# Performance work log

Hardware: AMD Instinct MI355X
Metric: run time of the kernel (lower is better)

## Reference

```python
import jax, jax.numpy as jnp
import numpy as np

C_SKIP = 64       # channels of a and of b (concat -> 128)
C_OUT = 64
N = 131072        # coarse nodes
E = 1048576       # directed edges (avg degree 8)
N_FINE = 4 * N    # fine mesh nodes after unpool
K = 3 * N_FINE    # unpool scatter assignments


def setup_inputs() -> dict:
    key = jax.random.key(0)
    ks = jax.random.split(key, 9)
    return {
        "a": jax.random.normal(ks[0], (C_SKIP, N), dtype=jnp.float32),
        "b": jax.random.normal(ks[1], (C_SKIP, N), dtype=jnp.float32),
        "W_self": jax.random.normal(ks[2], (C_OUT, 2 * C_SKIP), dtype=jnp.float32) * 0.05,
        "W_neigh": jax.random.normal(ks[3], (C_OUT, 2 * C_SKIP), dtype=jnp.float32) * 0.05,
        "bias": jax.random.normal(ks[4], (C_OUT,), dtype=jnp.float32) * 0.05,
        "gather_index": jax.random.randint(ks[5], (E,), 0, N),
        "reduce_index": jax.random.randint(ks[6], (E,), 0, N),
        "unpool_src": jax.random.randint(ks[7], (K,), 0, N),
        "unpool_dst": jax.random.randint(ks[8], (K,), 0, N_FINE),
    }


def reference(a, b, W_self, W_neigh, bias, gather_index, reduce_index, unpool_src, unpool_dst):
    # concat skip connection along channel dim (-2)
    x = jnp.concatenate((a, b), axis=-2)                  # [C_in, N]
    n = x.shape[-1]
    # GraphConv: gather source features along edges, segment-sum into targets
    msgs = x[:, gather_index]                              # [C_in, E]
    agg = jax.ops.segment_sum(msgs.T, reduce_index, num_segments=n).T  # [C_in, N]
    h = W_self @ x + W_neigh @ agg + bias[:, None]         # [C_out, N]
    h = jax.nn.relu(h)
    # GraphUnpool with reduce='amax': scatter-max coarse features to fine mesh
    out = jnp.zeros((h.shape[0], 4 * n), dtype=h.dtype)
    out = out.at[:, unpool_dst].max(h[:, unpool_src])      # [C_out, N_fine]
    return out
```

## Files before the change

### kernel.cpp

```cpp
#include <hip/hip_runtime.h>
#include <stdint.h>

constexpr int NN = 131072;
constexpr int EE = 1048576;
constexpr int NF = 4 * NN;
constexpr int KK = 3 * NF;

constexpr int NSB  = 256;
constexpr int TPS  = 1024;
constexpr int SHC_E = 9;
constexpr int SHC_K = 10;
constexpr int NBC_E = NN >> SHC_E;
constexpr int NBC_K = NF >> SHC_K;
constexpr int EPT_E = EE / NSB / TPS;
constexpr int EPT_K = KK / NSB / TPS;
constexpr int KOFF2 = NBC_E * NSB;
constexpr int NH2   = KOFF2 + NBC_K * NSB;
constexpr int NSCB  = NH2 / 2048;
constexpr int NTRB  = NN / 32 / 4;

constexpr int CAP_AG = 1024;
constexpr int CAP_UP = 896;

typedef __attribute__((ext_vector_type(8))) short bf16x8;
typedef __attribute__((ext_vector_type(4))) float f32x4;

__device__ inline uint32_t bf16rn(float f) {
    uint32_t u = __float_as_uint(f);
    return (u + 0x7FFFu + ((u >> 16) & 1u)) >> 16;
}
__device__ inline uint32_t pack2(float lo, float hi) {
    return bf16rn(lo) | (bf16rn(hi) << 16);
}
__device__ inline float bf_lo(uint32_t v) { return __uint_as_float(v << 16); }
__device__ inline float bf_hi(uint32_t v) { return __uint_as_float(v & 0xFFFF0000u); }

template<int NB, int EPT>
__device__ void pass1_body(const int* __restrict__ idx, int shift,
                           int* __restrict__ histG, int blk, int* hist)
{
    for (int f = threadIdx.x; f < NB; f += TPS) hist[f] = 0;
    __syncthreads();
    int base = blk * (TPS * EPT);
#pragma unroll
    for (int u = 0; u < EPT; ++u) {
        int b = idx[base + u * TPS + threadIdx.x] >> shift;
        atomicAdd(&hist[b], 1);
    }
    __syncthreads();
    for (int f = threadIdx.x; f < NB; f += TPS)
        histG[f * NSB + blk] = hist[f];
}

__global__ __launch_bounds__(1024) void k_fused1(
    const float* __restrict__ a, const float* __restrict__ b,
    uint32_t* __restrict__ xTb,
    const int* __restrict__ reduce_i, const int* __restrict__ up_dst,
    int* __restrict__ histG)
{
    __shared__ int smem[128 * 33];
    if (blockIdx.x < NTRB) {
        float (*tile)[33] = (float (*)[33])smem;
        for (int t = 0; t < 4; ++t) {
            int i0 = (blockIdx.x * 4 + t) * 32;
            for (int f = threadIdx.x; f < 128 * 32; f += TPS) {
                int c = f >> 5, j = f & 31;
                const float* src = (c < 64) ? a : b;
                tile[c][j] = src[(size_t)(c & 63) * NN + i0 + j];
            }
            __syncthreads();
            for (int f = threadIdx.x; f < 64 * 32; f += TPS) {
                int p = f & 63, j = f >> 6;
                xTb[(size_t)(i0 + j) * 64 + p] =
                    pack2(tile[2 * p][j], tile[2 * p + 1][j]);
            }
            __syncthreads();
        }
    } else if (blockIdx.x < NTRB + NSB) {
        pass1_body<NBC_E, EPT_E>(reduce_i, SHC_E, histG, blockIdx.x - NTRB, smem);
    } else {
        pass1_body<NBC_K, EPT_K>(up_dst, SHC_K, histG + KOFF2,
                                 blockIdx.x - NTRB - NSB, smem);
    }
}

__global__ __launch_bounds__(256) void k_bsum(
    const int* __restrict__ cnt, int* __restrict__ bsum)
{
    __shared__ int s[256];
    int base = blockIdx.x * 2048;
    int sum = 0;
    for (int j = threadIdx.x; j < 2048; j += 256) sum += cnt[base + j];
    s[threadIdx.x] = sum;
    __syncthreads();
    for (int o = 128; o > 0; o >>= 1) {
        if (threadIdx.x < o) s[threadIdx.x] += s[threadIdx.x + o];
        __syncthreads();
    }
    if (threadIdx.x == 0) bsum[blockIdx.x] = s[0];
}

__global__ __launch_bounds__(256) void k_final(
    int* __restrict__ offs, const int* __restrict__ bsum)
{
    __shared__ int ts[256];
    int partial = 0;
    for (int i = threadIdx.x; i < blockIdx.x; i += 256) partial += bsum[i];
    ts[threadIdx.x] = partial;
    __syncthreads();
    for (int o = 128; o > 0; o >>= 1) {
        if (threadIdx.x < o) ts[threadIdx.x] += ts[threadIdx.x + o];
        __syncthreads();
    }
    int bb = ts[0];
    __syncthreads();

    int base = blockIdx.x * 2048 + threadIdx.x * 8;
    int loc[8];
    int sum = 0;
#pragma unroll
    for (int u = 0; u < 8; ++u) {
        int v = offs[base + u];
        loc[u] = sum;
        sum += v;
    }
    ts[threadIdx.x] = sum;
    __syncthreads();
    for (int o = 1; o < 256; o <<= 1) {
        int v = (threadIdx.x >= o) ? ts[threadIdx.x - o] : 0;
        __syncthreads();
        ts[threadIdx.x] += v;
        __syncthreads();
    }
    int texc = (threadIdx.x == 0) ? 0 : ts[threadIdx.x - 1];
#pragma unroll
    for (int u = 0; u < 8; ++u) offs[base + u] = bb + texc + loc[u];
    if (blockIdx.x == gridDim.x - 1 && threadIdx.x == 255) offs[NH2] = bb + ts[255];
}

template<int NB, int EPT>
__device__ void pass2_body(const int* __restrict__ idx,
                           const int* __restrict__ payload, int shift,
                           const int* __restrict__ offsG, int sub,
                           uint32_t* __restrict__ pairs, int blk, int* curs)
{
    int lmask = (1 << shift) - 1;
    for (int f = threadIdx.x; f < NB; f += TPS)
        curs[f] = offsG[f * NSB + blk] - sub;
    __syncthreads();
    int base = blk * (TPS * EPT);
#pragma unroll
    for (int u = 0; u < EPT; ++u) {
        int e = base + u * TPS + threadIdx.x;
        int bk = idx[e];
        int pos = atomicAdd(&curs[bk >> shift], 1);
        pairs[pos] = (uint32_t)payload[e] | ((uint32_t)(bk & lmask) << 17);
    }
}

__global__ __launch_bounds__(1024) void k_pass2(
    const int* __restrict__ reduce_i, const int* __restrict__ gather_i,
    const int* __restrict__ up_dst, const int* __restrict__ up_src,
    const int* __restrict__ offs,
    uint32_t* __restrict__ pairsE, uint32_t* __restrict__ pairsK)
{
    __shared__ int curs[NBC_K];
    if (blockIdx.x < NSB)
        pass2_body<NBC_E, EPT_E>(reduce_i, gather_i, SHC_E, offs, 0,
                                 pairsE, blockIdx.x, curs);
    else
        pass2_body<NBC_K, EPT_K>(up_dst, up_src, SHC_K, offs + KOFF2, EE,
                                 pairsK, blockIdx.x - NSB, curs);
}

__global__ __launch_bounds__(256) void k_aggcsr(
    const uint32_t* __restrict__ xTb, const int* __restrict__ offs,
    const uint32_t* __restrict__ pairsE, uint32_t* __restrict__ aggB)
{
    __shared__ uint32_t stage[CAP_AG];
    __shared__ uint32_t list[CAP_AG];
    __shared__ int loffs[65];
    __shared__ int curs[64];
    __shared__ int nstage;
    int binc = blockIdx.x >> 3, sub = blockIdx.x & 7;
    int beg = offs[binc * NSB], end = offs[(binc + 1) * NSB];
    if (threadIdx.x == 0) nstage = 0;
    if (threadIdx.x < 64) curs[threadIdx.x] = 0;
    __syncthreads();
    int lane = threadIdx.x & 63;

    for (int i0 = beg; i0 < end; i0 += 256) {
        int i = i0 + threadIdx.x;
        bool mine = false;
        uint32_t ent = 0;
        if (i < end) {
            uint32_t u = pairsE[i];
            int loc = u >> 17;
            mine = (loc >> 6) == sub;
            ent = (u & 0x1FFFFu) | ((uint32_t)(loc & 63) << 17);
        }
        unsigned long long mask = __ballot(mine);
        if (mask) {
            int leader = __ffsll(mask) - 1;
            int rank = __popcll(mask & ((1ull << lane) - 1ull));
            int wb = 0;
            if (lane == leader) wb = atomicAdd(&nstage, (int)__popcll(mask));
            wb = __shfl(wb, leader);
            int p = wb + rank;
            if (mine && p < CAP_AG) stage[p] = ent;
        }
    }
    __syncthreads();
    int cnt = min(nstage, CAP_AG);
    for (int i = threadIdx.x; i < cnt; i += 256)
        atomicAdd(&curs[stage[i] >> 17], 1);
    __syncthreads();
    if (threadIdx.x == 0) {
        int run = 0;
        for (int j = 0; j < 64; ++j) {
            loffs[j] = run;
            run += curs[j];
            curs[j] = loffs[j];
        }
        loffs[64] = run;
    }
    __syncthreads();
    for (int i = threadIdx.x; i < cnt; i += 256) {
        uint32_t u = stage[i];
        int p = atomicAdd(&curs[u >> 17], 1);
        list[p] = u;
    }
    __syncthreads();

    int w = threadIdx.x >> 6;
    int n0 = w * 16, n1 = n0 + 16;
    int e0 = loffs[n0], e1 = loffs[n1];
    size_t rowbase = (size_t)(binc * 512 + sub * 64) * 64 + lane;
    float sx = 0.f, sy = 0.f;
    int cur = n0;
    for (int e = e0; e < e1; e += 16) {
        int nb = e1 - e;
        uint32_t pr[16], v[16];
#pragma unroll
        for (int j = 0; j < 16; ++j)
            pr[j] = list[e + ((j < nb) ? j : (nb - 1))];
#pragma unroll
        for (int j = 0; j < 16; ++j)
            v[j] = xTb[(size_t)(pr[j] & 0x1FFFF) * 64 + lane];
#pragma unroll
        for (int j = 0; j < 16; ++j) {
            if (j < nb) {
                int d = pr[j] >> 17;
                if (d != cur) {
                    aggB[rowbase + (size_t)cur * 64] = pack2(sx, sy);
                    for (int z = cur + 1; z < d; ++z)
                        aggB[rowbase + (size_t)z * 64] = 0u;
                    cur = d;
                    sx = 0.f; sy = 0.f;
                }
                sx += bf_lo(v[j]);
                sy += bf_hi(v[j]);
            }
        }
    }
    aggB[rowbase + (size_t)cur * 64] = pack2(sx, sy);
    for (int z = cur + 1; z < n1; ++z)
        aggB[rowbase + (size_t)z * 64] = 0u;
}

__global__ __launch_bounds__(256) void k_gemm(
    const uint32_t* __restrict__ xTb, const uint32_t* __restrict__ aggB,
    const float* __restrict__ Wself, const float* __restrict__ Wneigh,
    const float* __restrict__ bias, uint32_t* __restrict__ hT)
{
    int lane = threadIdx.x & 63;
    int wid = blockIdx.x * 4 + (threadIdx.x >> 6);
    int lr = lane & 15, lq = lane >> 4;

    bf16x8 wf[4][8];
#pragma unroll
    for (int mt = 0; mt < 4; ++mt) {
#pragma unroll
        for (int kt = 0; kt < 8; ++kt) {
            const float* W = (kt < 4) ? Wself : Wneigh;
            const float* p = W + (size_t)(mt * 16 + lr) * 128 + (kt & 3) * 32 + lq * 8;
            bf16x8 v;
#pragma unroll
            for (int j = 0; j < 8; ++j) v[j] = (short)bf16rn(p[j]);
            wf[mt][kt] = v;
        }
    }
    float bv[4][4];
#pragma unroll
    for (int mt = 0; mt < 4; ++mt)
#pragma unroll
        for (int r = 0; r < 4; ++r)
            bv[mt][r] = bias[mt * 16 + lq * 4 + r];

    const int NG = NN / 16;
    int stride = gridDim.x * 4;
    for (int g = wid; g < NG; g += stride) {
        int n = g * 16 + lr;
        const uint32_t* xr = xTb + (size_t)n * 64 + lq * 4;
        const uint32_t* ar = aggB + (size_t)n * 64 + lq * 4;
        bf16x8 bq[8];
#pragma unroll
        for (int kt = 0; kt < 4; ++kt)
            bq[kt] = *reinterpret_cast<const bf16x8*>(xr + kt * 16);
#pragma unroll
        for (int kt = 0; kt < 4; ++kt)
            bq[4 + kt] = *reinterpret_cast<const bf16x8*>(ar + kt * 16);
#pragma unroll
        for (int mt = 0; mt < 4; ++mt) {
            f32x4 acc = {0.f, 0.f, 0.f, 0.f};
#pragma unroll
            for (int kt = 0; kt < 8; ++kt)
                acc = __builtin_amdgcn_mfma_f32_16x16x32_bf16(wf[mt][kt], bq[kt], acc, 0, 0, 0);
            uint32_t u0 = pack2(fmaxf(acc[0] + bv[mt][0], 0.f), fmaxf(acc[1] + bv[mt][1], 0.f));
            uint32_t u1 = pack2(fmaxf(acc[2] + bv[mt][2], 0.f), fmaxf(acc[3] + bv[mt][3], 0.f));
            *reinterpret_cast<uint2*>(hT + (size_t)n * 32 + mt * 8 + lq * 2) = make_uint2(u0, u1);
        }
    }
}

__global__ __launch_bounds__(256) void k_unpoolcsr(
    const uint16_t* __restrict__ hT16, const int* __restrict__ offsK,
    const uint32_t* __restrict__ pairsK, float* __restrict__ out)
{
    __shared__ uint32_t stage[CAP_UP];
    __shared__ uint32_t list[CAP_UP];
    __shared__ int loffs[129];
    __shared__ int curs[128];
    __shared__ uint16_t buf[128][65];
    __shared__ int nstage;
    int binc = blockIdx.x >> 3, sub = blockIdx.x & 7;
    int beg = offsK[binc * NSB] - EE, end = offsK[(binc + 1) * NSB] - EE;
    if (threadIdx.x == 0) nstage = 0;
    if (threadIdx.x < 128) curs[threadIdx.x] = 0;
    for (int f = threadIdx.x; f < 128 * 65; f += 256) ((uint16_t*)buf)[f] = 0;
    __syncthreads();
    int lane = threadIdx.x & 63;

    for (int i0 = beg; i0 < end; i0 += 256) {
        int i = i0 + threadIdx.x;
        bool mine = false;
        uint32_t ent = 0;
        if (i < end) {
            uint32_t u = pairsK[i];
            int loc = u >> 17;
            mine = (loc >> 7) == sub;
            ent = (u & 0x1FFFFu) | ((uint32_t)(loc & 127) << 17);
        }
        unsigned long long mask = __ballot(mine);
        if (mask) {
            int leader = __ffsll(mask) - 1;
            int rank = __popcll(mask & ((1ull << lane) - 1ull));
            int wb = 0;
            if (lane == leader) wb = atomicAdd(&nstage, (int)__popcll(mask));
            wb = __shfl(wb, leader);
            int p = wb + rank;
            if (mine && p < CAP_UP) stage[p] = ent;
        }
    }
    __syncthreads();
    int cnt = min(nstage, CAP_UP);
    for (int i = threadIdx.x; i < cnt; i += 256)
        atomicAdd(&curs[stage[i] >> 17], 1);
    __syncthreads();
    if (threadIdx.x == 0) {
        int run = 0;
        for (int j = 0; j < 128; ++j) {
            loffs[j] = run;
            run += curs[j];
            curs[j] = loffs[j];
        }
        loffs[128] = run;
    }
    __syncthreads();
    for (int i = threadIdx.x; i < cnt; i += 256) {
        uint32_t u = stage[i];
        int p = atomicAdd(&curs[u >> 17], 1);
        list[p] = u;
    }
    __syncthreads();

    int w = threadIdx.x >> 6;
    int n0 = w * 32, n1 = n0 + 32;
    int e0 = loffs[n0], e1 = loffs[n1];
    uint32_t m = 0;
    int cur = n0;
    for (int e = e0; e < e1; e += 16) {
        int nb = e1 - e;
        uint32_t pr[16], v[16];
#pragma unroll
        for (int j = 0; j < 16; ++j)
            pr[j] = list[e + ((j < nb) ? j : (nb - 1))];
#pragma unroll
        for (int j = 0; j < 16; ++j)
            v[j] = hT16[(size_t)(pr[j] & 0x1FFFF) * 64 + lane];
#pragma unroll
        for (int j = 0; j < 16; ++j) {
            if (j < nb) {
                int d = pr[j] >> 17;
                if (d != cur) {
                    buf[cur][lane] = (uint16_t)m;
                    cur = d;
                    m = 0;
                }
                m = max(m, v[j]);
            }
        }
    }
    buf[cur][lane] = (uint16_t)m;
    __syncthreads();
    int j0 = binc * 1024 + sub * 128;
    for (int f = threadIdx.x; f < 64 * 128; f += 256) {
        int c = f >> 7, j = f & 127;
        out[(size_t)c * NF + j0 + j] = __uint_as_float(((uint32_t)buf[j][c]) << 16);
    }
}

extern "C" void kernel_launch(void* const* d_in, const int* in_sizes, int n_in,
                              void* d_out, int out_size, void* d_ws, size_t ws_size,
                              hipStream_t stream)
{
    const float* a      = (const float*)d_in[0];
    const float* b      = (const float*)d_in[1];
    const float* Wself  = (const float*)d_in[2];
    const float* Wneigh = (const float*)d_in[3];
    const float* bias   = (const float*)d_in[4];
    const int* gather_i = (const int*)d_in[5];
    const int* reduce_i = (const int*)d_in[6];
    const int* up_src   = (const int*)d_in[7];
    const int* up_dst   = (const int*)d_in[8];
    float* out = (float*)d_out;

    uint32_t* xTb   = (uint32_t*)d_ws;
    uint32_t* aggB  = xTb + (size_t)NN * 64;
    uint32_t* hT    = aggB + (size_t)NN * 64;
    uint32_t* pairsK= hT + (size_t)NN * 32;
    int* offs       = (int*)(pairsK + KK);
    int* bsum       = offs + (size_t)NH2 + 1;
    uint32_t* pairsE= hT;

    size_t need = ((size_t)NN * 160 + KK + (size_t)NH2 + 1 + NSCB) * 4;
    if (ws_size < need) return;

    k_fused1<<<NTRB + 2 * NSB, TPS, 0, stream>>>(a, b, xTb, reduce_i, up_dst, offs);

    k_bsum<<<NSCB, 256, 0, stream>>>(offs, bsum);
    k_final<<<NSCB, 256, 0, stream>>>(offs, bsum);

    k_pass2<<<2 * NSB, TPS, 0, stream>>>(reduce_i, gather_i, up_dst, up_src,
                                         offs, pairsE, pairsK);

    k_aggcsr<<<8 * NBC_E, 256, 0, stream>>>(xTb, offs, pairsE, aggB);

    k_gemm<<<512, 256, 0, stream>>>(xTb, aggB, Wself, Wneigh, bias, hT);

    k_unpoolcsr<<<8 * NBC_K, 256, 0, stream>>>((const uint16_t*)hT, offs + KOFF2,
                                               pairsK, out);
}
```

Before: 243.3 us.

## Add per-bucket node-level sort pass to build full CSR offsets

Adds a new k_pass3 kernel that sorts each coarse bucket's pairs by local node in place and writes global per-node offset arrays for both the edge and unpool lists. The aggregation and unpool kernels then read their node ranges directly from these offsets. Before, each of eight sub-blocks rescanned the whole bucket, filtered it with ballots and ran a serial single-thread prefix scan. This removes that eightfold redundant scanning and the per-block local sort, at the cost of one extra launch and more workspace for the offset arrays.

```diff
diff --git a/kernel.cpp b/kernel.cpp
--- a/kernel.cpp
+++ b/kernel.cpp
@@ -19,8 +19,8 @@
 constexpr int NSCB  = NH2 / 2048;
 constexpr int NTRB  = NN / 32 / 4;
 
-constexpr int CAP_AG = 1024;
-constexpr int CAP_UP = 896;
+constexpr int CAP3_E = 5120;
+constexpr int CAP3_K = 4096;
 
 typedef __attribute__((ext_vector_type(8))) short bf16x8;
 typedef __attribute__((ext_vector_type(4))) float f32x4;
@@ -173,77 +173,82 @@
                                  pairsK, blockIdx.x - NSB, curs);
 }
 
-__global__ __launch_bounds__(256) void k_aggcsr(
-    const uint32_t* __restrict__ xTb, const int* __restrict__ offs,
+template<int NB, int CAP>
+__device__ void pass3_body(uint32_t* __restrict__ pairs, int beg, int end,
+                           int* __restrict__ nodeOff, int nodeBase,
+                           bool last, int totalNode,
+                           uint32_t* list, int* curs, int* tmp)
+{
+    int tid = threadIdx.x;
+    int cnt = min(end - beg, CAP);
+    for (int i = tid; i < cnt; i += TPS) list[i] = pairs[beg + i];
+    if (tid < NB) curs[tid] = 0;
+    __syncthreads();
+    for (int i = tid; i < cnt; i += TPS) atomicAdd(&curs[list[i] >> 17], 1);
+    __syncthreads();
+    int own = (tid < NB) ? curs[tid] : 0;
+    if (tid < NB) tmp[tid] = own;
+    __syncthreads();
+    for (int o = 1; o < NB; o <<= 1) {
+        int v = (tid < NB && tid >= o) ? tmp[tid - o] : 0;
+        __syncthreads();
+        if (tid < NB) tmp[tid] += v;
+        __syncthreads();
+    }
+    if (tid < NB) {
+        int excl = tmp[tid] - own;
+        curs[tid] = excl;
+        nodeOff[nodeBase + tid] = beg + excl;
+    }
+    if (last && tid == 0) nodeOff[totalNode] = beg + cnt;
+    __syncthreads();
+    for (int i = tid; i < cnt; i += TPS) {
+        uint32_t u = list[i];
+        int p = atomicAdd(&curs[u >> 17], 1);
+        pairs[beg + p] = u;
+    }
+}
+
+__global__ __launch_bounds__(1024) void k_pass3(
+    const int* __restrict__ offs,
+    uint32_t* __restrict__ pairsE, uint32_t* __restrict__ pairsK,
+    int* __restrict__ nodeOffE, int* __restrict__ nodeOffK)
+{
+    __shared__ uint32_t list[CAP3_E];
+    __shared__ int curs[1024];
+    __shared__ int tmp[1024];
+    if (blockIdx.x < NBC_E) {
+        int b = blockIdx.x;
+        int beg = offs[b * NSB], end = offs[(b + 1) * NSB];
+        pass3_body<512, CAP3_E>(pairsE, beg, end, nodeOffE, b * 512,
+                                b == NBC_E - 1, NN, list, curs, tmp);
+    } else {
+        int b = blockIdx.x - NBC_E;
+        int beg = offs[KOFF2 + b * NSB] - EE;
+        int end = offs[KOFF2 + (b + 1) * NSB] - EE;
+        pass3_body<1024, CAP3_K>(pairsK, beg, end, nodeOffK, b * 1024,
+                                 b == NBC_K - 1, NF, list, curs, tmp);
+    }
+}
+
+__global__ __launch_bounds__(256) void k_agg2(
+    const uint32_t* __restrict__ xTb, const int* __restrict__ nodeOffE,
     const uint32_t* __restrict__ pairsE, uint32_t* __restrict__ aggB)
 {
-    __shared__ uint32_t stage[CAP_AG];
-    __shared__ uint32_t list[CAP_AG];
-    __shared__ int loffs[65];
-    __shared__ int curs[64];
-    __shared__ int nstage;
-    int binc = blockIdx.x >> 3, sub = blockIdx.x & 7;
-    int beg = offs[binc * NSB], end = offs[(binc + 1) * NSB];
-    if (threadIdx.x == 0) nstage = 0;
-    if (threadIdx.x < 64) curs[threadIdx.x] = 0;
-    __syncthreads();
-    int lane = threadIdx.x & 63;
-
-    for (int i0 = beg; i0 < end; i0 += 256) {
-        int i = i0 + threadIdx.x;
-        bool mine = false;
-        uint32_t ent = 0;
-        if (i < end) {
-            uint32_t u = pairsE[i];
-            int loc = u >> 17;
-            mine = (loc >> 6) == sub;
-            ent = (u & 0x1FFFFu) | ((uint32_t)(loc & 63) << 17);
-        }
-        unsigned long long mask = __ballot(mine);
-        if (mask) {
-            int leader = __ffsll(mask) - 1;
-            int rank = __popcll(mask & ((1ull << lane) - 1ull));
-            int wb = 0;
-            if (lane == leader) wb = atomicAdd(&nstage, (int)__popcll(mask));
-            wb = __shfl(wb, leader);
-            int p = wb + rank;
-            if (mine && p < CAP_AG) stage[p] = ent;
-        }
-    }
-    __syncthreads();
-    int cnt = min(nstage, CAP_AG);
-    for (int i = threadIdx.x; i < cnt; i += 256)
-        atomicAdd(&curs[stage[i] >> 17], 1);
-    __syncthreads();
-    if (threadIdx.x == 0) {
-        int run = 0;
-        for (int j = 0; j < 64; ++j) {
-            loffs[j] = run;
-            run += curs[j];
-            curs[j] = loffs[j];
-        }
-        loffs[64] = run;
-    }
-    __syncthreads();
-    for (int i = threadIdx.x; i < cnt; i += 256) {
-        uint32_t u = stage[i];
-        int p = atomicAdd(&curs[u >> 17], 1);
-        list[p] = u;
-    }
-    __syncthreads();
-
-    int w = threadIdx.x >> 6;
-    int n0 = w * 16, n1 = n0 + 16;
-    int e0 = loffs[n0], e1 = loffs[n1];
-    size_t rowbase = (size_t)(binc * 512 + sub * 64) * 64 + lane;
+    int w = threadIdx.x >> 6, lane = threadIdx.x & 63;
+    int n0g = blockIdx.x * 64 + w * 16;
+    int e0 = nodeOffE[n0g], e1 = nodeOffE[n0g + 16];
+    int curLoc = n0g & 511;
+    int curEnd = curLoc + 16;
+    int cbase = n0g - curLoc;
     float sx = 0.f, sy = 0.f;
-    int cur = n0;
+    int cur = curLoc;
     for (int e = e0; e < e1; e += 16) {
         int nb = e1 - e;
         uint32_t pr[16], v[16];
 #pragma unroll
         for (int j = 0; j < 16; ++j)
-            pr[j] = list[e + ((j < nb) ? j : (nb - 1))];
+            pr[j] = pairsE[e + ((j < nb) ? j : (nb - 1))];
 #pragma unroll
         for (int j = 0; j < 16; ++j)
             v[j] = xTb[(size_t)(pr[j] & 0x1FFFF) * 64 + lane];
@@ -252,9 +257,9 @@
             if (j < nb) {
                 int d = pr[j] >> 17;
                 if (d != cur) {
-                    aggB[rowbase + (size_t)cur * 64] = pack2(sx, sy);
+                    aggB[(size_t)(cbase + cur) * 64 + lane] = pack2(sx, sy);
                     for (int z = cur + 1; z < d; ++z)
-                        aggB[rowbase + (size_t)z * 64] = 0u;
+                        aggB[(size_t)(cbase + z) * 64 + lane] = 0u;
                     cur = d;
                     sx = 0.f; sy = 0.f;
                 }
@@ -263,9 +268,9 @@
             }
         }
     }
-    aggB[rowbase + (size_t)cur * 64] = pack2(sx, sy);
-    for (int z = cur + 1; z < n1; ++z)
-        aggB[rowbase + (size_t)z * 64] = 0u;
+    aggB[(size_t)(cbase + cur) * 64 + lane] = pack2(sx, sy);
+    for (int z = cur + 1; z < curEnd; ++z)
+        aggB[(size_t)(cbase + z) * 64 + lane] = 0u;
 }
 
 __global__ __launch_bounds__(256) void k_gemm(
@@ -323,85 +328,33 @@
     }
 }
 
-__global__ __launch_bounds__(256) void k_unpoolcsr(
-    const uint16_t* __restrict__ hT16, const int* __restrict__ offsK,
+__global__ __launch_bounds__(256) void k_unpool2(
+    const uint16_t* __restrict__ hT16, const int* __restrict__ nodeOffK,
     const uint32_t* __restrict__ pairsK, float* __restrict__ out)
 {
-    __shared__ uint32_t stage[CAP_UP];
-    __shared__ uint32_t list[CAP_UP];
-    __shared__ int loffs[129];
-    __shared__ int curs[128];
     __shared__ uint16_t buf[128][65];
-    __shared__ int nstage;
-    int binc = blockIdx.x >> 3, sub = blockIdx.x & 7;
-    int beg = offsK[binc * NSB] - EE, end = offsK[(binc + 1) * NSB] - EE;
-    if (threadIdx.x == 0) nstage = 0;
-    if (threadIdx.x < 128) curs[threadIdx.x] = 0;
+    int w = threadIdx.x >> 6, lane = threadIdx.x & 63;
+    int j0 = blockIdx.x * 128;
+    int lbase = j0 & 1023;
     for (int f = threadIdx.x; f < 128 * 65; f += 256) ((uint16_t*)buf)[f] = 0;
     __syncthreads();
-    int lane = threadIdx.x & 63;
-
-    for (int i0 = beg; i0 < end; i0 += 256) {
-        int i = i0 + threadIdx.x;
-        bool mine = false;
-        uint32_t ent = 0;
-        if (i < end) {
-            uint32_t u = pairsK[i];
-            int loc = u >> 17;
-            mine = (loc >> 7) == sub;
-            ent = (u & 0x1FFFFu) | ((uint32_t)(loc & 127) << 17);
-        }
-        unsigned long long mask = __ballot(mine);
-        if (mask) {
-            int leader = __ffsll(mask) - 1;
-            int rank = __popcll(mask & ((1ull << lane) - 1ull));
-            int wb = 0;
-            if (lane == leader) wb = atomicAdd(&nstage, (int)__popcll(mask));
-            wb = __shfl(wb, leader);
-            int p = wb + rank;
-            if (mine && p < CAP_UP) stage[p] = ent;
-        }
-    }
-    __syncthreads();
-    int cnt = min(nstage, CAP_UP);
-    for (int i = threadIdx.x; i < cnt; i += 256)
-        atomicAdd(&curs[stage[i] >> 17], 1);
-    __syncthreads();
-    if (threadIdx.x == 0) {
-        int run = 0;
-        for (int j = 0; j < 128; ++j) {
-            loffs[j] = run;
-            run += curs[j];
-            curs[j] = loffs[j];
-        }
-        loffs[128] = run;
-    }
-    __syncthreads();
-    for (int i = threadIdx.x; i < cnt; i += 256) {
-        uint32_t u = stage[i];
-        int p = atomicAdd(&curs[u >> 17], 1);
-        list[p] = u;
-    }
-    __syncthreads();
-
-    int w = threadIdx.x >> 6;
-    int n0 = w * 32, n1 = n0 + 32;
-    int e0 = loffs[n0], e1 = loffs[n1];
+    int n0 = j0 + w * 32;
+    int e0 = nodeOffK[n0], e1 = nodeOffK[n0 + 32];
     uint32_t m = 0;
-    int cur = n0;
+    int cur = (n0 & 1023) - lbase;
     for (int e = e0; e < e1; e += 16) {
         int nb = e1 - e;
         uint32_t pr[16], v[16];
 #pragma unroll
         for (int j = 0; j < 16; ++j)
-            pr[j] = list[e + ((j < nb) ? j : (nb - 1))];
+            pr[j] = pairsK[e + ((j < nb) ? j : (nb - 1))];
 #pragma unroll
         for (int j = 0; j < 16; ++j)
             v[j] = hT16[(size_t)(pr[j] & 0x1FFFF) * 64 + lane];
 #pragma unroll
         for (int j = 0; j < 16; ++j) {
             if (j < nb) {
-                int d = pr[j] >> 17;
+                int d = (int)(pr[j] >> 17) - lbase;
                 if (d != cur) {
                     buf[cur][lane] = (uint16_t)m;
                     cur = d;
@@ -413,7 +366,6 @@
     }
     buf[cur][lane] = (uint16_t)m;
     __syncthreads();
-    int j0 = binc * 1024 + sub * 128;
     for (int f = threadIdx.x; f < 64 * 128; f += 256) {
         int c = f >> 7, j = f & 127;
         out[(size_t)c * NF + j0 + j] = __uint_as_float(((uint32_t)buf[j][c]) << 16);
@@ -435,15 +387,18 @@
     const int* up_dst   = (const int*)d_in[8];
     float* out = (float*)d_out;
 
-    uint32_t* xTb   = (uint32_t*)d_ws;
-    uint32_t* aggB  = xTb + (size_t)NN * 64;
-    uint32_t* hT    = aggB + (size_t)NN * 64;
-    uint32_t* pairsK= hT + (size_t)NN * 32;
-    int* offs       = (int*)(pairsK + KK);
-    int* bsum       = offs + (size_t)NH2 + 1;
-    uint32_t* pairsE= hT;
-
-    size_t need = ((size_t)NN * 160 + KK + (size_t)NH2 + 1 + NSCB) * 4;
+    uint32_t* xTb    = (uint32_t*)d_ws;
+    uint32_t* aggB   = xTb + (size_t)NN * 64;
+    uint32_t* hT     = aggB + (size_t)NN * 64;
+    uint32_t* pairsK = hT + (size_t)NN * 32;
+    int* offs        = (int*)(pairsK + KK);
+    int* bsum        = offs + (size_t)NH2 + 1;
+    int* nodeOffE    = bsum + NSCB;
+    int* nodeOffK    = nodeOffE + NN + 1;
+    uint32_t* pairsE = hT;
+
+    size_t need = ((size_t)NN * 160 + KK + (size_t)NH2 + 1 + NSCB +
+                   (size_t)NN + 1 + (size_t)NF + 1) * 4;
     if (ws_size < need) return;
 
     k_fused1<<<NTRB + 2 * NSB, TPS, 0, stream>>>(a, b, xTb, reduce_i, up_dst, offs);
@@ -454,10 +409,13 @@
     k_pass2<<<2 * NSB, TPS, 0, stream>>>(reduce_i, gather_i, up_dst, up_src,
                                          offs, pairsE, pairsK);
 
-    k_aggcsr<<<8 * NBC_E, 256, 0, stream>>>(xTb, offs, pairsE, aggB);
+    k_pass3<<<NBC_E + NBC_K, TPS, 0, stream>>>(offs, pairsE, pairsK,
+                                               nodeOffE, nodeOffK);
+
+    k_agg2<<<NN / 64, 256, 0, stream>>>(xTb, nodeOffE, pairsE, aggB);
 
     k_gemm<<<512, 256, 0, stream>>>(xTb, aggB, Wself, Wneigh, bias, hT);
 
-    k_unpoolcsr<<<8 * NBC_K, 256, 0, stream>>>((const uint16_t*)hT, offs + KOFF2,
-                                               pairsK, out);
-}
+    k_unpool2<<<NF / 128, 256, 0, stream>>>((const uint16_t*)hT, nodeOffK,
+                                            pairsK, out);
+}
```

Result: no change. 245.6 us (+1.0%).
